# Kernel optimization log

Measured on AMD Instinct MI355X. Metric: run time of the kernel, lower is better.

The kernel has to match this reference:

```python
import jax, jax.numpy as jnp
import numpy as np
import math

B, S, H = 4, 2048, 1024
NH, HD = 16, 64
BASE = 10000.0

def _rope_cos_sin(seq_len, dim):
    inv_freq = 1.0 / (BASE ** (jnp.arange(0, dim, 2, dtype=jnp.float32) / dim))
    pos = jnp.arange(seq_len, dtype=jnp.float32)
    freqs = jnp.outer(pos, inv_freq)              # [S, dim/2]
    emb = jnp.concatenate([freqs, freqs], axis=-1)  # [S, dim]
    return jnp.cos(emb), jnp.sin(emb)

def _apply_rotary(x, cos, sin):
    # x: [B, NH, S, HD]; cos/sin: [S, HD]
    d = x.shape[-1] // 2
    x1, x2 = x[..., :d], x[..., d:]
    rotated = jnp.concatenate([-x2, x1], axis=-1)
    return x * cos[None, None] + rotated * sin[None, None]

def setup_inputs() -> dict:
    key = jax.random.key(0)
    ks = jax.random.split(key, 5)
    scale = 1.0 / math.sqrt(H)
    return {
        "x": jax.random.normal(ks[0], (B, S, H), dtype=jnp.float32),
        "attention_mask": jnp.ones((B, S), dtype=jnp.int32),
        "Wq": jax.random.normal(ks[1], (H, H), dtype=jnp.float32) * scale,
        "Wk": jax.random.normal(ks[2], (H, H), dtype=jnp.float32) * scale,
        "Wv": jax.random.normal(ks[3], (H, H), dtype=jnp.float32) * scale,
        "Wo": jax.random.normal(ks[4], (H, H), dtype=jnp.float32) * scale,
    }

def reference(x, attention_mask, Wq, Wk, Wv, Wo):
    b, s, _ = x.shape
    # projections (nn.Linear: x @ W.T)
    q = (x @ Wq.T).reshape(b, s, NH, HD).transpose(0, 2, 1, 3)  # [B,NH,S,HD]
    k = (x @ Wk.T).reshape(b, s, NH, HD).transpose(0, 2, 1, 3)
    v = (x @ Wv.T).reshape(b, s, NH, HD).transpose(0, 2, 1, 3)
    cos, sin = _rope_cos_sin(s, HD)
    q = _apply_rotary(q, cos, sin)
    k = _apply_rotary(k, cos, sin)
    scores = jnp.einsum('bhqd,bhkd->bhqk', q, k) / math.sqrt(HD)
    mask = attention_mask[:, None, None, :]  # [B,1,1,S]
    scores = jnp.where(mask == 0, -jnp.inf, scores)
    attn = jax.nn.softmax(scores, axis=-1)
    out = jnp.einsum('bhqk,bhkd->bhqd', attn, v)
    out = out.transpose(0, 2, 1, 3).reshape(b, s, NH * HD)
    return out @ Wo.T
```

## Files before the change

### kernel.cpp

```cpp
#include <hip/hip_runtime.h>
#include <hip/hip_bf16.h>

#define B_  4
#define S_  2048
#define H_  1024
#define NH_ 16
#define HD_ 64

typedef __bf16 bf16;
typedef __attribute__((ext_vector_type(8))) __bf16 bf16x8;
typedef __attribute__((ext_vector_type(4))) __bf16 bf16x4;
typedef __attribute__((ext_vector_type(4))) float f32x4;

typedef const __attribute__((address_space(1))) char* gptr_t;
typedef __attribute__((address_space(3))) char* lptr_t;
#define GLOAD_LDS16(g, l) __builtin_amdgcn_global_load_lds((gptr_t)(g), (lptr_t)(l), 16, 0, 0)

__device__ __forceinline__ f32x4 mfma16(bf16x8 a, bf16x8 b, f32x4 c) {
    return __builtin_amdgcn_mfma_f32_16x16x32_bf16(a, b, c, 0, 0, 0);
}

__device__ __forceinline__ void swz_bid(int& bx, int& by) {
    const int gx = gridDim.x;
    const int nwg = gx * gridDim.y;
    const int i = blockIdx.x + gx * blockIdx.y;
    const int w = (i & 7) * (nwg >> 3) + (i >> 3);
    bx = w % gx;
    by = w / gx;
}

__global__ void k_cvt(const float* __restrict__ src, bf16* __restrict__ dst, int n4) {
    int i = blockIdx.x * blockDim.x + threadIdx.x;
    if (i < n4) {
        float4 v = ((const float4*)src)[i];
        bf16x4 o;
        o[0] = (__bf16)v.x; o[1] = (__bf16)v.y; o[2] = (__bf16)v.z; o[3] = (__bf16)v.w;
        *(bf16x4*)(dst + i * 4) = o;
    }
}

__global__ void k_tab(float* __restrict__ cosT, float* __restrict__ sinT) {
    int i = blockIdx.x * blockDim.x + threadIdx.x;
    if (i >= S_ * 32) return;
    int s = i >> 5, d = i & 31;
    float inv = powf(10000.0f, -(float)d * (1.0f / 32.0f));
    float ang = (float)s * inv;
    cosT[i] = cosf(ang);
    sinT[i] = sinf(ang);
}

template<int EPI>
__global__ __launch_bounds__(256) void k_gemm(
        const bf16* __restrict__ A, const bf16* __restrict__ Bw,
        bf16* __restrict__ q_out, bf16* __restrict__ k_out, bf16* __restrict__ v_out,
        const float* __restrict__ cosT, const float* __restrict__ sinT,
        float* __restrict__ fout) {
    __shared__ bf16 As[128 * 32];
    __shared__ bf16 Bs[128 * 32];
    const int t = threadIdx.x, l = t & 63, w = t >> 6;
    const int lr = l & 15, hi = l >> 4;
    int bx, by;
    swz_bid(bx, by);
    const int m0 = by * 128, n0 = bx * 128;
    const int wr = (w >> 1) * 64, wc = (w & 1) * 64;
    f32x4 acc[4][4] = {};

    for (int k0 = 0; k0 < 1024; k0 += 32) {
        __syncthreads();
#pragma unroll
        for (int i = 0; i < 2; ++i) {
            int o = i * 4096 + t * 16;
            int row = o >> 6, colb = o & 63;
            GLOAD_LDS16((const char*)A + ((size_t)(m0 + row) * 1024 + k0) * 2 + colb,
                        (char*)As + o);
            GLOAD_LDS16((const char*)Bw + ((size_t)(n0 + row) * 1024 + k0) * 2 + colb,
                        (char*)Bs + o);
        }
        __syncthreads();
        bf16x8 af[4], bfr[4];
#pragma unroll
        for (int mi = 0; mi < 4; ++mi)
            af[mi] = *(const bf16x8*)&As[(wr + mi * 16 + lr) * 32 + hi * 8];
#pragma unroll
        for (int ni = 0; ni < 4; ++ni)
            bfr[ni] = *(const bf16x8*)&Bs[(wc + ni * 16 + lr) * 32 + hi * 8];
#pragma unroll
        for (int mi = 0; mi < 4; ++mi)
#pragma unroll
            for (int ni = 0; ni < 4; ++ni)
                acc[mi][ni] = mfma16(af[mi], bfr[ni], acc[mi][ni]);
    }

    if (EPI == 0) {
        const int nbase = n0 + wc;
        const int which = nbase >> 10;
        const int head = (nbase & 1023) >> 6;
        if (which == 2) {
#pragma unroll
            for (int mi = 0; mi < 4; ++mi) {
                int m = m0 + wr + mi * 16 + hi * 4;
                int bb = m >> 11, s = m & 2047;
                int st = s & 63;
                int pos = ((st >> 5) & 1) * 32 + ((st >> 2) & 3) * 8 + ((st >> 4) & 1) * 4;
                int sp = (s & ~63) | pos;
                size_t vbase = (size_t)(bb * NH_ + head) * HD_;
#pragma unroll
                for (int ni = 0; ni < 4; ++ni) {
                    bf16x4 o;
#pragma unroll
                    for (int r = 0; r < 4; ++r) o[r] = (__bf16)acc[mi][ni][r];
                    *(bf16x4*)(v_out + (vbase + ni * 16 + lr) * (size_t)S_ + sp) = o;
                }
            }
        } else {
            bf16* dst = which == 0 ? q_out : k_out;
            const float qsc = which == 0 ? 0.125f * 1.4426950408889634f : 1.0f;
#pragma unroll
            for (int mi = 0; mi < 4; ++mi) {
#pragma unroll
                for (int r = 0; r < 4; ++r) {
                    int m = m0 + wr + mi * 16 + hi * 4 + r;
                    int bb = m >> 11, s = m & 2047;
                    size_t base = (((size_t)bb * NH_ + head) * S_ + s) * HD_;
#pragma unroll
                    for (int ni = 0; ni < 2; ++ni) {
                        int d = ni * 16 + lr;
                        float c = cosT[s * 32 + d] * qsc, sn = sinT[s * 32 + d] * qsc;
                        float x1 = acc[mi][ni][r], x2 = acc[mi][ni + 2][r];
                        dst[base + d]      = (__bf16)(x1 * c - x2 * sn);
                        dst[base + d + 32] = (__bf16)(x2 * c + x1 * sn);
                    }
                }
            }
        }
    } else {
#pragma unroll
        for (int mi = 0; mi < 4; ++mi)
#pragma unroll
            for (int ni = 0; ni < 4; ++ni)
#pragma unroll
                for (int r = 0; r < 4; ++r)
                    fout[(size_t)(m0 + wr + mi * 16 + hi * 4 + r) * 1024
                         + (n0 + wc + ni * 16 + lr)] = acc[mi][ni][r];
    }
}

__global__ __launch_bounds__(512, 4) void k_attn(
        const bf16* __restrict__ qr, const bf16* __restrict__ kr,
        const bf16* __restrict__ vt, const int* __restrict__ mask,
        bf16* __restrict__ aout) {
    __shared__ bf16 Ks[2][64 * 64];
    __shared__ bf16 Vs[2][64 * 64];
    const int t = threadIdx.x, l = t & 63, w = t >> 6;
    const int lr = l & 15, hi = l >> 4;
    const int sw = (lr & 7) << 4;
    int bx, by;
    swz_bid(bx, by);
    const int bh = by, b = bh >> 4, head = bh & 15;
    const int qbase = bx * 256 + w * 32;

    const bf16* Qb = qr + (size_t)bh * S_ * HD_;
    const char* Kg = (const char*)(kr + (size_t)bh * S_ * HD_);
    const char* Vg = (const char*)(vt + (size_t)bh * HD_ * S_);
    const int* mrow = mask + b * S_;

    bf16x8 qf[2][2];
#pragma unroll
    for (int qh = 0; qh < 2; ++qh)
#pragma unroll
        for (int h = 0; h < 2; ++h)
            qf[qh][h] = *(const bf16x8*)(Qb + (size_t)(qbase + qh * 16 + lr) * HD_ + h * 32 + hi * 8);

    bf16x8 onesf;
#pragma unroll
    for (int j = 0; j < 8; ++j) onesf[j] = (__bf16)1.0f;

    int anyz0 = 0;
    for (int i = l; i < S_ / 4; i += 64) {
        int4 m4 = ((const int4*)mrow)[i];
        anyz0 |= (m4.x == 0) | (m4.y == 0) | (m4.z == 0) | (m4.w == 0);
    }
    const bool anyz = __any(anyz0);

    f32x4 acc[4][2] = {};
    f32x4 accL[2] = {};

    auto STAGE = [&](int buf, int kv0) {
        int o = t * 16;
        int row = o >> 7, colb = o & 127;
        int scol = colb ^ ((row & 7) << 4);
        GLOAD_LDS16(Kg + (size_t)(kv0 + row) * 128 + scol, (char*)Ks[buf] + o);
        GLOAD_LDS16(Vg + (size_t)row * (S_ * 2) + (size_t)kv0 * 2 + scol,
                    (char*)Vs[buf] + o);
    };

    auto TILE = [&](int buf, int kv0) {
        const char* Kc = (const char*)Ks[buf];
        const char* Vc = (const char*)Vs[buf];

        f32x4 st[4][2] = {};
#pragma unroll
        for (int g = 0; g < 4; ++g) {
            int rb = (g * 16 + lr) * 128;
            bf16x8 kf0 = *(const bf16x8*)(Kc + rb + ((hi * 16) ^ sw));
            bf16x8 kf1 = *(const bf16x8*)(Kc + rb + ((64 + hi * 16) ^ sw));
            st[g][0] = mfma16(kf0, qf[0][0], st[g][0]);
            st[g][0] = mfma16(kf1, qf[0][1], st[g][0]);
            st[g][1] = mfma16(kf0, qf[1][0], st[g][1]);
            st[g][1] = mfma16(kf1, qf[1][1], st[g][1]);
        }

        if (anyz) {
#pragma unroll
            for (int g = 0; g < 4; ++g) {
                int4 mv = *(const int4*)(mrow + kv0 + g * 16 + hi * 4);
#pragma unroll
                for (int qh = 0; qh < 2; ++qh) {
                    st[g][qh][0] = mv.x ? st[g][qh][0] : -INFINITY;
                    st[g][qh][1] = mv.y ? st[g][qh][1] : -INFINITY;
                    st[g][qh][2] = mv.z ? st[g][qh][2] : -INFINITY;
                    st[g][qh][3] = mv.w ? st[g][qh][3] : -INFINITY;
                }
            }
        }

        bf16x8 pB[2][2];
#pragma unroll
        for (int qh = 0; qh < 2; ++qh)
#pragma unroll
            for (int g = 0; g < 4; ++g)
#pragma unroll
                for (int r = 0; r < 4; ++r)
                    pB[qh][g >> 1][(g & 1) * 4 + r] =
                        (__bf16)__builtin_exp2f(st[g][qh][r]);

        accL[0] = mfma16(onesf, pB[0][0], accL[0]);
        accL[0] = mfma16(onesf, pB[0][1], accL[0]);
        accL[1] = mfma16(onesf, pB[1][0], accL[1]);
        accL[1] = mfma16(onesf, pB[1][1], accL[1]);
#pragma unroll
        for (int dt = 0; dt < 4; ++dt) {
            const char* vrow = Vc + (dt * 16 + lr) * 128;
#pragma unroll
            for (int ks = 0; ks < 2; ++ks) {
                bf16x8 vf = *(const bf16x8*)(vrow + ((ks * 64 + hi * 16) ^ sw));
                acc[dt][0] = mfma16(vf, pB[0][ks], acc[dt][0]);
                acc[dt][1] = mfma16(vf, pB[1][ks], acc[dt][1]);
            }
        }
    };

    STAGE(0, 0);
    const int NT = S_ / 64;
    for (int ti = 0; ti < NT; ti += 2) {
        __syncthreads();
        if (ti + 1 < NT) STAGE(1, (ti + 1) * 64);
        TILE(0, ti * 64);
        __syncthreads();
        if (ti + 2 < NT) STAGE(0, (ti + 2) * 64);
        TILE(1, (ti + 1) * 64);
    }

    float inv[2] = {1.0f / accL[0][0], 1.0f / accL[1][0]};
#pragma unroll
    for (int qh = 0; qh < 2; ++qh) {
        size_t obase = ((size_t)(b * S_ + qbase + qh * 16 + lr)) * H_ + head * HD_;
#pragma unroll
        for (int dt = 0; dt < 4; ++dt) {
            bf16x4 o;
#pragma unroll
            for (int r = 0; r < 4; ++r) o[r] = (__bf16)(acc[dt][qh][r] * inv[qh]);
            *(bf16x4*)(aout + obase + dt * 16 + hi * 4) = o;
        }
    }
}

extern "C" void kernel_launch(void* const* d_in, const int* in_sizes, int n_in,
                              void* d_out, int out_size, void* d_ws, size_t ws_size,
                              hipStream_t stream) {
    const float* x  = (const float*)d_in[0];
    const int* mask = (const int*)d_in[1];
    const float* Wq = (const float*)d_in[2];
    const float* Wk = (const float*)d_in[3];
    const float* Wv = (const float*)d_in[4];
    const float* Wo = (const float*)d_in[5];
    float* out = (float*)d_out;

    char* ws = (char*)d_ws;
    bf16* xb    = (bf16*)ws;
    bf16* wqkv  = (bf16*)(ws + (size_t)16 * 1048576);
    bf16* wob   = (bf16*)(ws + (size_t)22 * 1048576);
    bf16* qr    = (bf16*)(ws + (size_t)24 * 1048576);
    bf16* kr    = (bf16*)(ws + (size_t)40 * 1048576);
    bf16* vtw   = (bf16*)(ws + (size_t)56 * 1048576);
    float* cosT = (float*)(ws + (size_t)72 * 1048576);
    float* sinT = (float*)(ws + (size_t)72 * 1048576 + 262144);

    k_cvt<<<2097152 / 256, 256, 0, stream>>>(x, xb, 2097152);
    k_cvt<<<262144 / 256, 256, 0, stream>>>(Wq, wqkv, 262144);
    k_cvt<<<262144 / 256, 256, 0, stream>>>(Wk, wqkv + 1048576, 262144);
    k_cvt<<<262144 / 256, 256, 0, stream>>>(Wv, wqkv + 2097152, 262144);
    k_cvt<<<262144 / 256, 256, 0, stream>>>(Wo, wob, 262144);
    k_tab<<<256, 256, 0, stream>>>(cosT, sinT);

    k_gemm<0><<<dim3(24, 64), 256, 0, stream>>>(xb, wqkv, qr, kr, vtw, cosT, sinT, nullptr);

    k_attn<<<dim3(8, 64), 512, 0, stream>>>(qr, kr, vtw, mask, xb);

    k_gemm<1><<<dim3(8, 64), 256, 0, stream>>>(xb, wob, nullptr, nullptr, nullptr,
                                               nullptr, nullptr, out);
}
```

Measured before the change: 220.8 us.

## Double GEMM K-tile to 64 with XOR-swizzled LDS and merge weight conversions

The GEMM now stages a K=64 slice per iteration instead of 32. Global-to-LDS loads are placed with an XOR swizzle on the column chunk, and the fragment reads apply the same swizzle. This halves the number of barrier pairs per K loop and is meant to avoid LDS bank conflicts on the 128-byte rows, at the cost of twice the LDS per block. The four weight-conversion launches are also merged into a single kernel to cut launch overhead.

```diff
diff --git a/kernel.cpp b/kernel.cpp
--- a/kernel.cpp
+++ b/kernel.cpp
@@ -37,6 +37,20 @@
         o[0] = (__bf16)v.x; o[1] = (__bf16)v.y; o[2] = (__bf16)v.z; o[3] = (__bf16)v.w;
         *(bf16x4*)(dst + i * 4) = o;
     }
+}
+
+__global__ void k_cvtw(const float* __restrict__ Wq, const float* __restrict__ Wk,
+                       const float* __restrict__ Wv, const float* __restrict__ Wo,
+                       bf16* __restrict__ wqkv, bf16* __restrict__ wob) {
+    int i = blockIdx.x * blockDim.x + threadIdx.x;
+    int region = i >> 18;
+    int j = i & 262143;
+    const float* src = region == 0 ? Wq : region == 1 ? Wk : region == 2 ? Wv : Wo;
+    bf16* dst = region < 3 ? wqkv + (size_t)region * 1048576 : wob;
+    float4 v = ((const float4*)src)[j];
+    bf16x4 o;
+    o[0] = (__bf16)v.x; o[1] = (__bf16)v.y; o[2] = (__bf16)v.z; o[3] = (__bf16)v.w;
+    *(bf16x4*)(dst + j * 4) = o;
 }
 
 __global__ void k_tab(float* __restrict__ cosT, float* __restrict__ sinT) {
@@ -55,40 +69,47 @@
         bf16* __restrict__ q_out, bf16* __restrict__ k_out, bf16* __restrict__ v_out,
         const float* __restrict__ cosT, const float* __restrict__ sinT,
         float* __restrict__ fout) {
-    __shared__ bf16 As[128 * 32];
-    __shared__ bf16 Bs[128 * 32];
+    __shared__ bf16 As[128 * 64];
+    __shared__ bf16 Bs[128 * 64];
     const int t = threadIdx.x, l = t & 63, w = t >> 6;
     const int lr = l & 15, hi = l >> 4;
+    const int sw = (lr & 7) << 4;
     int bx, by;
     swz_bid(bx, by);
     const int m0 = by * 128, n0 = bx * 128;
     const int wr = (w >> 1) * 64, wc = (w & 1) * 64;
     f32x4 acc[4][4] = {};
 
-    for (int k0 = 0; k0 < 1024; k0 += 32) {
+    for (int k0 = 0; k0 < 1024; k0 += 64) {
         __syncthreads();
 #pragma unroll
-        for (int i = 0; i < 2; ++i) {
+        for (int i = 0; i < 4; ++i) {
             int o = i * 4096 + t * 16;
-            int row = o >> 6, colb = o & 63;
-            GLOAD_LDS16((const char*)A + ((size_t)(m0 + row) * 1024 + k0) * 2 + colb,
+            int row = o >> 7, colb = o & 127;
+            int scol = colb ^ ((row & 7) << 4);
+            GLOAD_LDS16((const char*)A + ((size_t)(m0 + row) * 1024 + k0) * 2 + scol,
                         (char*)As + o);
-            GLOAD_LDS16((const char*)Bw + ((size_t)(n0 + row) * 1024 + k0) * 2 + colb,
+            GLOAD_LDS16((const char*)Bw + ((size_t)(n0 + row) * 1024 + k0) * 2 + scol,
                         (char*)Bs + o);
         }
         __syncthreads();
-        bf16x8 af[4], bfr[4];
-#pragma unroll
-        for (int mi = 0; mi < 4; ++mi)
-            af[mi] = *(const bf16x8*)&As[(wr + mi * 16 + lr) * 32 + hi * 8];
-#pragma unroll
-        for (int ni = 0; ni < 4; ++ni)
-            bfr[ni] = *(const bf16x8*)&Bs[(wc + ni * 16 + lr) * 32 + hi * 8];
-#pragma unroll
-        for (int mi = 0; mi < 4; ++mi)
+#pragma unroll
+        for (int kk = 0; kk < 2; ++kk) {
+            bf16x8 af[4], bfr[4];
+#pragma unroll
+            for (int mi = 0; mi < 4; ++mi)
+                af[mi] = *(const bf16x8*)((const char*)As
+                          + (wr + mi * 16 + lr) * 128 + ((kk * 64 + hi * 16) ^ sw));
 #pragma unroll
             for (int ni = 0; ni < 4; ++ni)
-                acc[mi][ni] = mfma16(af[mi], bfr[ni], acc[mi][ni]);
+                bfr[ni] = *(const bf16x8*)((const char*)Bs
+                          + (wc + ni * 16 + lr) * 128 + ((kk * 64 + hi * 16) ^ sw));
+#pragma unroll
+            for (int mi = 0; mi < 4; ++mi)
+#pragma unroll
+                for (int ni = 0; ni < 4; ++ni)
+                    acc[mi][ni] = mfma16(af[mi], bfr[ni], acc[mi][ni]);
+        }
     }
 
     if (EPI == 0) {
@@ -297,10 +318,7 @@
     float* sinT = (float*)(ws + (size_t)72 * 1048576 + 262144);
 
     k_cvt<<<2097152 / 256, 256, 0, stream>>>(x, xb, 2097152);
-    k_cvt<<<262144 / 256, 256, 0, stream>>>(Wq, wqkv, 262144);
-    k_cvt<<<262144 / 256, 256, 0, stream>>>(Wk, wqkv + 1048576, 262144);
-    k_cvt<<<262144 / 256, 256, 0, stream>>>(Wv, wqkv + 2097152, 262144);
-    k_cvt<<<262144 / 256, 256, 0, stream>>>(Wo, wob, 262144);
+    k_cvtw<<<1048576 / 256, 256, 0, stream>>>(Wq, Wk, Wv, Wo, wqkv, wob);
     k_tab<<<256, 256, 0, stream>>>(cosT, sinT);
 
     k_gemm<0><<<dim3(24, 64), 256, 0, stream>>>(xb, wqkv, qr, kr, vtw, cosT, sinT, nullptr);
```

Result: faster. 207.4 us (-6.1%).
